# Optimization experiments

Hardware: AMD Instinct MI355X
Metric: run time of the kernel (lower is better)

Reference implementation:

```python
import jax, jax.numpy as jnp
import numpy as np

N = 50000
IN_C, HID_C, OUT_C = 128, 256, 128
E = 800000


def sage_conv(x, edge_index, W_l, b_l, W_r, num_nodes):
    # PyG SAGEConv (aggr='mean'): out = lin_l(mean_{j in N(i)} x_j) + lin_r(x_i)
    src, dst = edge_index[0], edge_index[1]
    msgs = x[src]  # [E, C] gather of source features
    agg = jax.ops.segment_sum(msgs, dst, num_segments=num_nodes)  # [N, C]
    deg = jax.ops.segment_sum(jnp.ones((edge_index.shape[1],), x.dtype), dst,
                              num_segments=num_nodes)
    mean = agg / jnp.maximum(deg, 1.0)[:, None]
    return mean @ W_l.T + b_l + x @ W_r.T


def setup_inputs() -> dict:
    key = jax.random.key(0)
    ks = jax.random.split(key, 8)
    x = jax.random.normal(ks[0], (N, IN_C), dtype=jnp.float32)
    edge_index = jax.random.randint(ks[1], (2, E), 0, N, dtype=jnp.int64)
    s1 = 1.0 / np.sqrt(IN_C)
    s2 = 1.0 / np.sqrt(HID_C)
    W1_l = jax.random.uniform(ks[2], (HID_C, IN_C), jnp.float32, -s1, s1)
    W1_r = jax.random.uniform(ks[3], (HID_C, IN_C), jnp.float32, -s1, s1)
    b1 = jnp.zeros((HID_C,), jnp.float32)
    W2_l = jax.random.uniform(ks[4], (OUT_C, HID_C), jnp.float32, -s2, s2)
    W2_r = jax.random.uniform(ks[5], (OUT_C, HID_C), jnp.float32, -s2, s2)
    b2 = jnp.zeros((OUT_C,), jnp.float32)
    return {"x": x, "edge_index": edge_index,
            "W1_l": W1_l, "b1": b1, "W1_r": W1_r,
            "W2_l": W2_l, "b2": b2, "W2_r": W2_r}


def reference(x, edge_index, W1_l, b1, W1_r, W2_l, b2, W2_r):
    h = sage_conv(x, edge_index, W1_l, b1, W1_r, N)
    h = jax.nn.relu(h)
    # dropout p=0.5 is identity in eval mode (inference reference)
    out = sage_conv(h, edge_index, W2_l, b2, W2_r, N)
    return out
```

## Files before the change

kernel.cpp:

```cpp
#include <hip/hip_runtime.h>

#define NN   50000
#define INC  128
#define HIDC 256
#define OUTC 128
#define NE   800000
#define MP   50048
#define CAP  64

#define EPB 4096
#define NCH ((NE + EPB - 1) / EPB)
#define RSZ 6250
#define FILLB (NCH * 8)

typedef short bfrag __attribute__((ext_vector_type(8)));
typedef float f32x4 __attribute__((ext_vector_type(4)));
typedef float f4 __attribute__((ext_vector_type(4)));
typedef unsigned short us8 __attribute__((ext_vector_type(8)));

__device__ inline unsigned short f2b(float f) {
    union { float f; unsigned u; } v; v.f = f;
    unsigned u = v.u;
    return (unsigned short)((u + 0x7fffu + ((u >> 16) & 1u)) >> 16);
}
__device__ inline float b2f(unsigned short s) {
    union { unsigned u; float f; } v; v.u = ((unsigned)s) << 16;
    return v.f;
}

__global__ __launch_bounds__(256) void k_prefill(
    const float* __restrict__ x, const int* __restrict__ ei,
    const float* __restrict__ W1l, const float* __restrict__ W1r,
    const float* __restrict__ W2l, const float* __restrict__ W2r,
    unsigned short* __restrict__ xb16, unsigned short* __restrict__ A1f,
    unsigned short* __restrict__ B1f, unsigned short* __restrict__ B2f,
    int* __restrict__ cnt, unsigned short* __restrict__ csr) {
    const int b = blockIdx.x;
    if (b < FILLB) {
        const int r = b & 7;
        const int c = b >> 3;
        const int lo = r * RSZ, hi = lo + RSZ;
        const int base = c * EPB + threadIdx.x;
#pragma unroll
        for (int i = 0; i < EPB / 256; ++i) {
            int e = base + i * 256;
            if (e < NE) {
                int dst = __builtin_nontemporal_load(ei + NE + e);
                if (dst >= lo && dst < hi) {
                    int srcv = __builtin_nontemporal_load(ei + e);
                    int old = atomicAdd(&cnt[dst], 1);
                    if (old < CAP) csr[dst * CAP + old] = (unsigned short)srcv;
                }
            }
        }
        return;
    }
    const int pb = b - FILLB;
    if (pb < 3125) {
        int t = pb * 256 + threadIdx.x;
        int i = t >> 4;
        int c8 = t & 15;
        const float* src = x + (size_t)i * INC + c8 * 8;
        f4 v0 = __builtin_nontemporal_load((const f4*)src);
        f4 v1 = __builtin_nontemporal_load((const f4*)(src + 4));
        us8 o = { f2b(v0.x), f2b(v0.y), f2b(v0.z), f2b(v0.w),
                  f2b(v1.x), f2b(v1.y), f2b(v1.z), f2b(v1.w) };
        __builtin_nontemporal_store(o, (us8*)(xb16 + (size_t)i * INC + c8 * 8));
        size_t off = (size_t)(i >> 4) * 4096 + (size_t)(4 + (c8 >> 2)) * 512
                   + (size_t)(c8 & 3) * 128 + (size_t)(i & 15) * 8;
        __builtin_nontemporal_store(o, (us8*)(A1f + off));
    } else if (pb < 3157) {
        int t = (pb - 3125) * 256 + threadIdx.x;
        int n = t >> 5;
        int k8 = t & 31;
        int k = k8 * 8;
        const float* src = (k < 128) ? (W1l + (size_t)n * INC + k)
                                     : (W1r + (size_t)n * INC + (k - 128));
        f4 v0 = __builtin_nontemporal_load((const f4*)src);
        f4 v1 = __builtin_nontemporal_load((const f4*)(src + 4));
        us8 o = { f2b(v0.x), f2b(v0.y), f2b(v0.z), f2b(v0.w),
                  f2b(v1.x), f2b(v1.y), f2b(v1.z), f2b(v1.w) };
        size_t off = (size_t)(n >> 4) * 4096 + (size_t)(k8 >> 2) * 512
                   + (size_t)(k8 & 3) * 128 + (size_t)(n & 15) * 8;
        __builtin_nontemporal_store(o, (us8*)(B1f + off));
    } else {
        int t = (pb - 3157) * 256 + threadIdx.x;
        int n = t >> 5;
        int k8 = t & 31;
        const float* src = (n < 128) ? (W2l + (size_t)n * HIDC + k8 * 8)
                                     : (W2r + (size_t)(n - 128) * HIDC + k8 * 8);
        f4 v0 = __builtin_nontemporal_load((const f4*)src);
        f4 v1 = __builtin_nontemporal_load((const f4*)(src + 4));
        us8 o = { f2b(v0.x), f2b(v0.y), f2b(v0.z), f2b(v0.w),
                  f2b(v1.x), f2b(v1.y), f2b(v1.z), f2b(v1.w) };
        size_t off = (size_t)(n >> 4) * 4096 + (size_t)(k8 >> 2) * 512
                   + (size_t)(k8 & 3) * 128 + (size_t)(n & 15) * 8;
        __builtin_nontemporal_store(o, (us8*)(B2f + off));
    }
}

__global__ __launch_bounds__(256) void k_gather_mean(
    const int* __restrict__ cnt, const unsigned short* __restrict__ csr,
    const unsigned short* __restrict__ xb16, unsigned short* __restrict__ A1f) {
    const int node = blockIdx.x * 4 + (threadIdx.x >> 6);
    const int lane = threadIdx.x & 63;
    const int sub = lane >> 4;
    const int cl = lane & 15;
    const int cn = cnt[node];
    const int m = (cn < CAP) ? cn : CAP;
    const unsigned short* cb = csr + node * CAP;
    float acc[8] = {};
    const unsigned short* xb = xb16 + cl * 8;
    int i = sub;
    for (; i + 12 < m; i += 16) {
        int s0 = cb[i], s1 = cb[i + 4], s2 = cb[i + 8], s3 = cb[i + 12];
        us8 v0 = *(const us8*)(xb + (size_t)s0 * INC);
        us8 v1 = *(const us8*)(xb + (size_t)s1 * INC);
        us8 v2 = *(const us8*)(xb + (size_t)s2 * INC);
        us8 v3 = *(const us8*)(xb + (size_t)s3 * INC);
#pragma unroll
        for (int j = 0; j < 8; ++j)
            acc[j] += (b2f(v0[j]) + b2f(v1[j])) + (b2f(v2[j]) + b2f(v3[j]));
    }
    if (i + 4 < m) {
        int s0 = cb[i], s1 = cb[i + 4];
        us8 v0 = *(const us8*)(xb + (size_t)s0 * INC);
        us8 v1 = *(const us8*)(xb + (size_t)s1 * INC);
#pragma unroll
        for (int j = 0; j < 8; ++j) acc[j] += b2f(v0[j]) + b2f(v1[j]);
        i += 8;
    }
    if (i < m) {
        int s0 = cb[i];
        us8 v0 = *(const us8*)(xb + (size_t)s0 * INC);
#pragma unroll
        for (int j = 0; j < 8; ++j) acc[j] += b2f(v0[j]);
    }
#pragma unroll
    for (int j = 0; j < 8; ++j) {
        acc[j] += __shfl_xor(acc[j], 16, 64);
        acc[j] += __shfl_xor(acc[j], 32, 64);
    }
    if (sub == 0) {
        float inv = 1.0f / fmaxf((float)cn, 1.0f);
        us8 o;
#pragma unroll
        for (int j = 0; j < 8; ++j) o[j] = f2b(acc[j] * inv);
        size_t off = (size_t)(node >> 4) * 4096 + (size_t)(cl >> 2) * 512
                   + (size_t)(cl & 3) * 128 + (size_t)(node & 15) * 8;
        *(us8*)(A1f + off) = o;
    }
}

__global__ __launch_bounds__(256) void k_mgemm_fused(
    const unsigned short* __restrict__ A, const unsigned short* __restrict__ B1,
    const float* __restrict__ b1, const unsigned short* __restrict__ B2,
    const float* __restrict__ b2, unsigned short* __restrict__ HP,
    float* __restrict__ OUT) {
    __shared__ unsigned short Hsl[16384];
    const int tid = threadIdx.x;
    const int lane = tid & 63;
    const int w = tid >> 6;
    const int col = lane & 15, quad = lane >> 4;
    const int m0 = blockIdx.x * 64;

    {
        const us8* src = (const us8*)(A + (size_t)(m0 >> 4) * 4096);
        us8* dst = (us8*)Hsl;
#pragma unroll
        for (int i = 0; i < 8; ++i) dst[tid + i * 256] = src[tid + i * 256];
    }
    __syncthreads();

    f32x4 acc[4][4];
#pragma unroll
    for (int i = 0; i < 4; ++i)
#pragma unroll
        for (int j = 0; j < 4; ++j) acc[i][j] = (f32x4){0.f, 0.f, 0.f, 0.f};
#pragma unroll
    for (int kc = 0; kc < 8; ++kc) {
        bfrag a[4], b[4];
#pragma unroll
        for (int mt = 0; mt < 4; ++mt)
            a[mt] = *(const bfrag*)(Hsl + mt * 4096 + kc * 512 + quad * 128 + col * 8);
#pragma unroll
        for (int nt = 0; nt < 4; ++nt)
            b[nt] = *(const bfrag*)(B1 + (size_t)(w * 4 + nt) * 4096 + kc * 512 + quad * 128 + col * 8);
#pragma unroll
        for (int mt = 0; mt < 4; ++mt)
#pragma unroll
            for (int nt = 0; nt < 4; ++nt)
                acc[mt][nt] = __builtin_amdgcn_mfma_f32_16x16x32_bf16(a[mt], b[nt], acc[mt][nt], 0, 0, 0);
    }
    __syncthreads();

#pragma unroll
    for (int nt = 0; nt < 4; ++nt) {
        int n = w * 64 + nt * 16 + col;
        float bb = b1[n];
        int noff = (n >> 5) * 512 + ((n >> 3) & 3) * 128 + (n & 7);
#pragma unroll
        for (int mt = 0; mt < 4; ++mt) {
#pragma unroll
            for (int r = 0; r < 4; ++r) {
                int ml = quad * 4 + r;
                Hsl[mt * 4096 + noff + ml * 8] = f2b(fmaxf(acc[mt][nt][r] + bb, 0.f));
            }
        }
    }
    __syncthreads();

#pragma unroll
    for (int i = 0; i < 4; ++i)
#pragma unroll
        for (int j = 0; j < 4; ++j) acc[i][j] = (f32x4){0.f, 0.f, 0.f, 0.f};
#pragma unroll
    for (int kc = 0; kc < 8; ++kc) {
        bfrag a[4], b[4];
#pragma unroll
        for (int mt = 0; mt < 4; ++mt)
            a[mt] = *(const bfrag*)(Hsl + mt * 4096 + kc * 512 + quad * 128 + col * 8);
#pragma unroll
        for (int nt = 0; nt < 4; ++nt)
            b[nt] = *(const bfrag*)(B2 + (size_t)(w * 4 + nt) * 4096 + kc * 512 + quad * 128 + col * 8);
#pragma unroll
        for (int mt = 0; mt < 4; ++mt)
#pragma unroll
            for (int nt = 0; nt < 4; ++nt)
                acc[mt][nt] = __builtin_amdgcn_mfma_f32_16x16x32_bf16(a[mt], b[nt], acc[mt][nt], 0, 0, 0);
    }

    if (w < 2) {
#pragma unroll
        for (int mt = 0; mt < 4; ++mt)
#pragma unroll
            for (int nt = 0; nt < 4; ++nt) {
                int n = w * 64 + nt * 16 + col;
#pragma unroll
                for (int r = 0; r < 4; ++r) {
                    int m = m0 + mt * 16 + quad * 4 + r;
                    if (m < NN) HP[(size_t)m * OUTC + n] = f2b(acc[mt][nt][r]);
                }
            }
    } else {
#pragma unroll
        for (int mt = 0; mt < 4; ++mt)
#pragma unroll
            for (int nt = 0; nt < 4; ++nt) {
                int n = (w - 2) * 64 + nt * 16 + col;
                float bb = b2[n];
#pragma unroll
                for (int r = 0; r < 4; ++r) {
                    int m = m0 + mt * 16 + quad * 4 + r;
                    if (m < NN) OUT[(size_t)m * OUTC + n] = acc[mt][nt][r] + bb;
                }
            }
    }
}

__global__ __launch_bounds__(256) void k_gather_add(
    const int* __restrict__ cnt, const unsigned short* __restrict__ csr,
    const unsigned short* __restrict__ hp, float* __restrict__ out) {
    const int node = blockIdx.x * 4 + (threadIdx.x >> 6);
    const int lane = threadIdx.x & 63;
    const int sub = lane >> 4;
    const int cl = lane & 15;
    const int cn = cnt[node];
    const int m = (cn < CAP) ? cn : CAP;
    const unsigned short* cb = csr + node * CAP;
    float acc[8] = {};
    const unsigned short* hb = hp + cl * 8;
    int i = sub;
    for (; i + 12 < m; i += 16) {
        int s0 = cb[i], s1 = cb[i + 4], s2 = cb[i + 8], s3 = cb[i + 12];
        us8 v0 = *(const us8*)(hb + (size_t)s0 * OUTC);
        us8 v1 = *(const us8*)(hb + (size_t)s1 * OUTC);
        us8 v2 = *(const us8*)(hb + (size_t)s2 * OUTC);
        us8 v3 = *(const us8*)(hb + (size_t)s3 * OUTC);
#pragma unroll
        for (int j = 0; j < 8; ++j)
            acc[j] += (b2f(v0[j]) + b2f(v1[j])) + (b2f(v2[j]) + b2f(v3[j]));
    }
    if (i + 4 < m) {
        int s0 = cb[i], s1 = cb[i + 4];
        us8 v0 = *(const us8*)(hb + (size_t)s0 * OUTC);
        us8 v1 = *(const us8*)(hb + (size_t)s1 * OUTC);
#pragma unroll
        for (int j = 0; j < 8; ++j) acc[j] += b2f(v0[j]) + b2f(v1[j]);
        i += 8;
    }
    if (i < m) {
        int s0 = cb[i];
        us8 v0 = *(const us8*)(hb + (size_t)s0 * OUTC);
#pragma unroll
        for (int j = 0; j < 8; ++j) acc[j] += b2f(v0[j]);
    }
#pragma unroll
    for (int j = 0; j < 8; ++j) {
        acc[j] += __shfl_xor(acc[j], 16, 64);
        acc[j] += __shfl_xor(acc[j], 32, 64);
    }
    if (sub == 0) {
        float inv = 1.0f / fmaxf((float)cn, 1.0f);
        float* p = out + (size_t)node * OUTC + cl * 8;
        float4 c0v = *(float4*)p;
        float4 c1v = *(float4*)(p + 4);
        c0v.x += acc[0] * inv; c0v.y += acc[1] * inv;
        c0v.z += acc[2] * inv; c0v.w += acc[3] * inv;
        c1v.x += acc[4] * inv; c1v.y += acc[5] * inv;
        c1v.z += acc[6] * inv; c1v.w += acc[7] * inv;
        *(float4*)p = c0v;
        *(float4*)(p + 4) = c1v;
    }
}

extern "C" void kernel_launch(void* const* d_in, const int* in_sizes, int n_in,
                              void* d_out, int out_size, void* d_ws, size_t ws_size,
                              hipStream_t stream) {
    const float* x   = (const float*)d_in[0];
    const int*   ei  = (const int*)d_in[1];
    const float* W1l = (const float*)d_in[2];
    const float* b1  = (const float*)d_in[3];
    const float* W1r = (const float*)d_in[4];
    const float* W2l = (const float*)d_in[5];
    const float* b2  = (const float*)d_in[6];
    const float* W2r = (const float*)d_in[7];
    float* out = (float*)d_out;

    int* cnt = (int*)d_ws;
    unsigned short* csr = (unsigned short*)(cnt + ((NN + 63) & ~63));
    unsigned short* A1f  = csr + (size_t)NN * CAP;
    unsigned short* xb16 = A1f + (size_t)MP * 256;
    unsigned short* hp   = xb16 + (size_t)NN * 128;
    unsigned short* B1f  = hp + (size_t)NN * 128;
    unsigned short* B2f  = B1f + 256 * 256;

    (void)hipMemsetAsync(cnt, 0, (size_t)NN * sizeof(int), stream);

    k_prefill<<<FILLB + 3189, 256, 0, stream>>>(x, ei, W1l, W1r, W2l, W2r,
                                                xb16, A1f, B1f, B2f, cnt, csr);
    k_gather_mean<<<NN / 4, 256, 0, stream>>>(cnt, csr, xb16, A1f);

    k_mgemm_fused<<<MP / 64, 256, 0, stream>>>(A1f, B1f, b1, B2f, b2, hp, out);

    k_gather_add<<<NN / 4, 256, 0, stream>>>(cnt, csr, hp, out);
}
```

Measured before the change: 230.1 us.

## Fuse layer-1 neighbor mean gather into the fused GEMM kernel via LDS

Removes the separate gather-mean kernel and the A1f global staging buffer. Each GEMM block now loads its 64 rows of bf16 x directly into shared memory and computes the neighbor means for those rows in place before the MFMA stage. This saves a kernel launch and a global write plus read of the 50048x256 bf16 activation tile. In exchange, each block runs 16 serial gather iterations per wave before its GEMM, with far fewer blocks than the old gather kernel, which may reduce latency hiding for the irregular gathers.

```diff
diff --git a/kernel.cpp b/kernel.cpp
--- a/kernel.cpp
+++ b/kernel.cpp
@@ -32,9 +32,9 @@
     const float* __restrict__ x, const int* __restrict__ ei,
     const float* __restrict__ W1l, const float* __restrict__ W1r,
     const float* __restrict__ W2l, const float* __restrict__ W2r,
-    unsigned short* __restrict__ xb16, unsigned short* __restrict__ A1f,
-    unsigned short* __restrict__ B1f, unsigned short* __restrict__ B2f,
-    int* __restrict__ cnt, unsigned short* __restrict__ csr) {
+    unsigned short* __restrict__ xb16, unsigned short* __restrict__ B1f,
+    unsigned short* __restrict__ B2f, int* __restrict__ cnt,
+    unsigned short* __restrict__ csr) {
     const int b = blockIdx.x;
     if (b < FILLB) {
         const int r = b & 7;
@@ -66,9 +66,6 @@
         us8 o = { f2b(v0.x), f2b(v0.y), f2b(v0.z), f2b(v0.w),
                   f2b(v1.x), f2b(v1.y), f2b(v1.z), f2b(v1.w) };
         __builtin_nontemporal_store(o, (us8*)(xb16 + (size_t)i * INC + c8 * 8));
-        size_t off = (size_t)(i >> 4) * 4096 + (size_t)(4 + (c8 >> 2)) * 512
-                   + (size_t)(c8 & 3) * 128 + (size_t)(i & 15) * 8;
-        __builtin_nontemporal_store(o, (us8*)(A1f + off));
     } else if (pb < 3157) {
         int t = (pb - 3125) * 256 + threadIdx.x;
         int n = t >> 5;
@@ -99,64 +96,12 @@
     }
 }
 
-__global__ __launch_bounds__(256) void k_gather_mean(
+__global__ __launch_bounds__(256) void k_mgemm_fused(
     const int* __restrict__ cnt, const unsigned short* __restrict__ csr,
-    const unsigned short* __restrict__ xb16, unsigned short* __restrict__ A1f) {
-    const int node = blockIdx.x * 4 + (threadIdx.x >> 6);
-    const int lane = threadIdx.x & 63;
-    const int sub = lane >> 4;
-    const int cl = lane & 15;
-    const int cn = cnt[node];
-    const int m = (cn < CAP) ? cn : CAP;
-    const unsigned short* cb = csr + node * CAP;
-    float acc[8] = {};
-    const unsigned short* xb = xb16 + cl * 8;
-    int i = sub;
-    for (; i + 12 < m; i += 16) {
-        int s0 = cb[i], s1 = cb[i + 4], s2 = cb[i + 8], s3 = cb[i + 12];
-        us8 v0 = *(const us8*)(xb + (size_t)s0 * INC);
-        us8 v1 = *(const us8*)(xb + (size_t)s1 * INC);
-        us8 v2 = *(const us8*)(xb + (size_t)s2 * INC);
-        us8 v3 = *(const us8*)(xb + (size_t)s3 * INC);
-#pragma unroll
-        for (int j = 0; j < 8; ++j)
-            acc[j] += (b2f(v0[j]) + b2f(v1[j])) + (b2f(v2[j]) + b2f(v3[j]));
-    }
-    if (i + 4 < m) {
-        int s0 = cb[i], s1 = cb[i + 4];
-        us8 v0 = *(const us8*)(xb + (size_t)s0 * INC);
-        us8 v1 = *(const us8*)(xb + (size_t)s1 * INC);
-#pragma unroll
-        for (int j = 0; j < 8; ++j) acc[j] += b2f(v0[j]) + b2f(v1[j]);
-        i += 8;
-    }
-    if (i < m) {
-        int s0 = cb[i];
-        us8 v0 = *(const us8*)(xb + (size_t)s0 * INC);
-#pragma unroll
-        for (int j = 0; j < 8; ++j) acc[j] += b2f(v0[j]);
-    }
-#pragma unroll
-    for (int j = 0; j < 8; ++j) {
-        acc[j] += __shfl_xor(acc[j], 16, 64);
-        acc[j] += __shfl_xor(acc[j], 32, 64);
-    }
-    if (sub == 0) {
-        float inv = 1.0f / fmaxf((float)cn, 1.0f);
-        us8 o;
-#pragma unroll
-        for (int j = 0; j < 8; ++j) o[j] = f2b(acc[j] * inv);
-        size_t off = (size_t)(node >> 4) * 4096 + (size_t)(cl >> 2) * 512
-                   + (size_t)(cl & 3) * 128 + (size_t)(node & 15) * 8;
-        *(us8*)(A1f + off) = o;
-    }
-}
-
-__global__ __launch_bounds__(256) void k_mgemm_fused(
-    const unsigned short* __restrict__ A, const unsigned short* __restrict__ B1,
-    const float* __restrict__ b1, const unsigned short* __restrict__ B2,
-    const float* __restrict__ b2, unsigned short* __restrict__ HP,
-    float* __restrict__ OUT) {
+    const unsigned short* __restrict__ xb16,
+    const unsigned short* __restrict__ B1, const float* __restrict__ b1,
+    const unsigned short* __restrict__ B2, const float* __restrict__ b2,
+    unsigned short* __restrict__ HP, float* __restrict__ OUT) {
     __shared__ unsigned short Hsl[16384];
     const int tid = threadIdx.x;
     const int lane = tid & 63;
@@ -164,11 +109,70 @@
     const int col = lane & 15, quad = lane >> 4;
     const int m0 = blockIdx.x * 64;
 
-    {
-        const us8* src = (const us8*)(A + (size_t)(m0 >> 4) * 4096);
-        us8* dst = (us8*)Hsl;
-#pragma unroll
-        for (int i = 0; i < 8; ++i) dst[tid + i * 256] = src[tid + i * 256];
+#pragma unroll
+    for (int it = 0; it < 4; ++it) {
+        int idx = tid + it * 256;
+        int row = idx >> 4;
+        int c8 = idx & 15;
+        int gr = m0 + row; if (gr >= NN) gr = NN - 1;
+        us8 v = *(const us8*)(xb16 + (size_t)gr * INC + c8 * 8);
+        int off = (row >> 4) * 4096 + (4 + (c8 >> 2)) * 512 + (c8 & 3) * 128
+                + (row & 15) * 8;
+        *(us8*)(Hsl + off) = v;
+    }
+
+    const int sub = quad;
+    for (int t = 0; t < 16; ++t) {
+        const int nl = w * 16 + t;
+        const int node = m0 + nl;
+        int cn = 0, mdeg = 0;
+        const unsigned short* cb = csr;
+        if (node < NN) {
+            cn = cnt[node];
+            mdeg = (cn < CAP) ? cn : CAP;
+            cb = csr + node * CAP;
+        }
+        float acc[8] = {};
+        const unsigned short* xb = xb16 + col * 8;
+        int i = sub;
+        for (; i + 12 < mdeg; i += 16) {
+            int s0 = cb[i], s1 = cb[i + 4], s2 = cb[i + 8], s3 = cb[i + 12];
+            us8 v0 = *(const us8*)(xb + (size_t)s0 * INC);
+            us8 v1 = *(const us8*)(xb + (size_t)s1 * INC);
+            us8 v2 = *(const us8*)(xb + (size_t)s2 * INC);
+            us8 v3 = *(const us8*)(xb + (size_t)s3 * INC);
+#pragma unroll
+            for (int j = 0; j < 8; ++j)
+                acc[j] += (b2f(v0[j]) + b2f(v1[j])) + (b2f(v2[j]) + b2f(v3[j]));
+        }
+        if (i + 4 < mdeg) {
+            int s0 = cb[i], s1 = cb[i + 4];
+            us8 v0 = *(const us8*)(xb + (size_t)s0 * INC);
+            us8 v1 = *(const us8*)(xb + (size_t)s1 * INC);
+#pragma unroll
+            for (int j = 0; j < 8; ++j) acc[j] += b2f(v0[j]) + b2f(v1[j]);
+            i += 8;
+        }
+        if (i < mdeg) {
+            int s0 = cb[i];
+            us8 v0 = *(const us8*)(xb + (size_t)s0 * INC);
+#pragma unroll
+            for (int j = 0; j < 8; ++j) acc[j] += b2f(v0[j]);
+        }
+#pragma unroll
+        for (int j = 0; j < 8; ++j) {
+            acc[j] += __shfl_xor(acc[j], 16, 64);
+            acc[j] += __shfl_xor(acc[j], 32, 64);
+        }
+        if (sub == 0) {
+            float inv = 1.0f / fmaxf((float)cn, 1.0f);
+            us8 o;
+#pragma unroll
+            for (int j = 0; j < 8; ++j) o[j] = f2b(acc[j] * inv);
+            int off = (nl >> 4) * 4096 + (col >> 2) * 512 + (col & 3) * 128
+                    + (nl & 15) * 8;
+            *(us8*)(Hsl + off) = o;
+        }
     }
     __syncthreads();
 
@@ -329,8 +333,7 @@
 
     int* cnt = (int*)d_ws;
     unsigned short* csr = (unsigned short*)(cnt + ((NN + 63) & ~63));
-    unsigned short* A1f  = csr + (size_t)NN * CAP;
-    unsigned short* xb16 = A1f + (size_t)MP * 256;
+    unsigned short* xb16 = csr + (size_t)NN * CAP;
     unsigned short* hp   = xb16 + (size_t)NN * 128;
     unsigned short* B1f  = hp + (size_t)NN * 128;
     unsigned short* B2f  = B1f + 256 * 256;
@@ -338,10 +341,8 @@
     (void)hipMemsetAsync(cnt, 0, (size_t)NN * sizeof(int), stream);
 
     k_prefill<<<FILLB + 3189, 256, 0, stream>>>(x, ei, W1l, W1r, W2l, W2r,
-                                                xb16, A1f, B1f, B2f, cnt, csr);
-    k_gather_mean<<<NN / 4, 256, 0, stream>>>(cnt, csr, xb16, A1f);
-
-    k_mgemm_fused<<<MP / 64, 256, 0, stream>>>(A1f, B1f, b1, B2f, b2, hp, out);
-
+                                                xb16, B1f, B2f, cnt, csr);
+    k_mgemm_fused<<<MP / 64, 256, 0, stream>>>(cnt, csr, xb16, B1f, b1,
+                                               B2f, b2, hp, out);
     k_gather_add<<<NN / 4, 256, 0, stream>>>(cnt, csr, hp, out);
 }
```

Result: slower. 262.5 us (+14.1%).
